# Kernel optimization log

Measured on AMD Instinct MI355X. Metric: run time of the kernel, lower is better.

## Reference

```python
import jax, jax.numpy as jnp
import numpy as np

COS_EPS = 1e-6
LN_EPS = 1e-5

def _cosine_sim(a, b):
    # PyTorch F.cosine_similarity(dim=1, eps): dot / (max(||a||,eps)*max(||b||,eps))
    dot = jnp.sum(a * b, axis=1)
    na = jnp.maximum(jnp.linalg.norm(a, axis=1), COS_EPS)
    nb = jnp.maximum(jnp.linalg.norm(b, axis=1), COS_EPS)
    return dot / (na * nb)

def _layer_norm(x, gamma, beta):
    mu = jnp.mean(x, axis=-1, keepdims=True)
    var = jnp.mean(jnp.square(x - mu), axis=-1, keepdims=True)
    return (x - mu) * jax.lax.rsqrt(var + LN_EPS) * gamma + beta

def setup_inputs() -> dict:
    B, I, H = 8192, 1024, 1024
    key = jax.random.key(0)
    ks = jax.random.split(key, 10)
    s_in = 1.0 / np.sqrt(I + H)
    s_im = 1.0 / np.sqrt(I)
    return {
        "x": jax.random.normal(ks[0], (B, I), jnp.float32),
        "hx": jax.random.normal(ks[1], (B, H), jnp.float32),
        "cx": jax.random.normal(ks[2], (B, H), jnp.float32),
        # main gate linear: [I+H, 4H]
        "W": jax.random.uniform(ks[3], (I + H, 4 * H), jnp.float32, -s_in, s_in),
        "b": jax.random.uniform(ks[4], (4 * H,), jnp.float32, -s_in, s_in),
        # input_mapped: [I, H]
        "Wm": jax.random.uniform(ks[5], (I, H), jnp.float32, -s_im, s_im),
        "bm": jax.random.uniform(ks[6], (H,), jnp.float32, -s_im, s_im),
        # 4 LayerNorms (i, f, g, o)
        "gammas": 1.0 + 0.1 * jax.random.normal(ks[7], (4, H), jnp.float32),
        "betas": 0.1 * jax.random.normal(ks[8], (4, H), jnp.float32),
    }

def reference(x, hx, cx, W, b, Wm, bm, gammas, betas):
    H = hx.shape[1]
    # cosine attention gate between mapped input and hidden state
    input_mapped = x @ Wm + bm                                   # [B, H]
    attn = jax.nn.sigmoid(_cosine_sim(input_mapped, hx))[:, None]  # [B, 1]
    x_mod = x + attn * x
    gates = jnp.concatenate([x_mod, hx], axis=1) @ W + b         # [B, 4H]
    i_g, f_g, g_g, o_g = jnp.split(gates, 4, axis=1)
    i_g = jax.nn.sigmoid(_layer_norm(i_g, gammas[0], betas[0]))
    f_g = jax.nn.sigmoid(_layer_norm(f_g, gammas[1], betas[1]))
    g_g = jnp.tanh(_layer_norm(g_g, gammas[2], betas[2]))
    o_g = jax.nn.sigmoid(_layer_norm(o_g, gammas[3], betas[3]))
    cx_new = f_g * cx + i_g * g_g
    hx_new = o_g * jnp.tanh(cx_new)
    gate_co = jax.nn.sigmoid((_cosine_sim(hx_new, cx_new)[:, None] + 1.0) / 2.0)
    hx_modulated = hx_new + hx_new * gate_co
    return (hx_modulated, cx_new)
```

## Files before the change

### kernel.cpp

```cpp
#include <hip/hip_runtime.h>
#include <hip/hip_bf16.h>

#define DEV __device__ __forceinline__

typedef unsigned short u16;
typedef unsigned int u32;
typedef __attribute__((ext_vector_type(8))) short bf16x8;
typedef __attribute__((ext_vector_type(4))) float f32x4;

DEV float bf2f(u16 v) { u32 u = ((u32)v) << 16; return __builtin_bit_cast(float, u); }
DEV u16 f2bf(float f) {
    u32 u = __builtin_bit_cast(u32, f);
    u32 r = (u + 0x7fffu + ((u >> 16) & 1u)) >> 16;
    return (u16)r;
}
DEV float lo16(u32 u) { return __builtin_bit_cast(float, u << 16); }
DEV float hi16(u32 u) { return __builtin_bit_cast(float, u & 0xffff0000u); }
DEV float sigm(float x) { return 1.f / (1.f + __expf(-x)); }
DEV float clamp4(float v) { return fminf(fmaxf(v, -1e4f), 1e4f); }
DEV float loadf(const void* p, size_t i, int isf) {
    return isf ? clamp4(((const float*)p)[i]) : clamp4(bf2f(((const u16*)p)[i]));
}
DEV void load8(const void* p, size_t off, int isf, float* o) {
    if (isf) {
        const float* s = (const float*)p + off;
#pragma unroll
        for (int e = 0; e < 8; ++e) o[e] = clamp4(s[e]);
    } else {
        uint4 q = *(const uint4*)((const u16*)p + off);
        o[0] = clamp4(lo16(q.x)); o[1] = clamp4(hi16(q.x));
        o[2] = clamp4(lo16(q.y)); o[3] = clamp4(hi16(q.y));
        o[4] = clamp4(lo16(q.z)); o[5] = clamp4(hi16(q.z));
        o[6] = clamp4(lo16(q.w)); o[7] = clamp4(hi16(q.w));
    }
}
DEV uint4 pack8(const float* a) {
    uint4 q;
    q.x = (u32)f2bf(a[0]) | ((u32)f2bf(a[1]) << 16);
    q.y = (u32)f2bf(a[2]) | ((u32)f2bf(a[3]) << 16);
    q.z = (u32)f2bf(a[4]) | ((u32)f2bf(a[5]) << 16);
    q.w = (u32)f2bf(a[6]) | ((u32)f2bf(a[7]) << 16);
    return q;
}
DEV void store8(void* p, size_t off, int isf, const float* a) {
    if (isf) {
        float* d = (float*)p + off;
        *(float4*)(d) = (float4){a[0], a[1], a[2], a[3]};
        *(float4*)(d + 4) = (float4){a[4], a[5], a[6], a[7]};
    } else {
        *(uint4*)((u16*)p + off) = pack8(a);
    }
}

DEV void gload16(const void* g, void* l) {
    __builtin_amdgcn_global_load_lds(
        (const __attribute__((address_space(1))) void*)g,
        (__attribute__((address_space(3))) void*)l, 16, 0, 0);
}

__global__ void detect_dtype(const u32* __restrict__ xw, u32* __restrict__ flag) {
    const int lane = threadIdx.x & 63;
    int cnt = 0;
    for (int k = 0; k < 32; ++k) {
        u32 e = (xw[lane + 64 * k] >> 7) & 0xff;
        cnt += (e >= 118 && e <= 130) ? 1 : 0;
    }
#pragma unroll
    for (int off = 32; off > 0; off >>= 1) cnt += __shfl_xor(cnt, off, 64);
    if (lane == 0) *flag = (cnt > 1024) ? 0u : 1u;
}

__global__ __launch_bounds__(256) void cvt_bf16(const void* __restrict__ src,
                                                u16* __restrict__ dst, int n8,
                                                const u32* __restrict__ flagp) {
    const int isf = (int)*flagp;
    int i = blockIdx.x * 256 + threadIdx.x;
    if (i >= n8) return;
    size_t off = (size_t)i * 8;
    float a[8];
    load8(src, off, isf, a);
    *(uint4*)(dst + off) = pack8(a);
}

__global__ __launch_bounds__(256) void tr_any(const void* __restrict__ src,
                                              u16* __restrict__ dst,
                                              int R, int C,
                                              const u32* __restrict__ flagp) {
    const int isf = (int)*flagp;
    __shared__ __align__(16) u16 t[32][33];
    int tx = threadIdx.x & 31, ty = threadIdx.x >> 5;
    int c0 = blockIdx.x * 32, r0 = blockIdx.y * 32;
#pragma unroll
    for (int i = 0; i < 32; i += 8)
        t[ty + i][tx] = f2bf(loadf(src, (size_t)(r0 + ty + i) * C + (c0 + tx), isf));
    __syncthreads();
#pragma unroll
    for (int i = 0; i < 32; i += 8)
        dst[(size_t)(c0 + ty + i) * R + (r0 + tx)] = t[tx][ty + i];
}

__global__ __launch_bounds__(256) void gemm_bt(
    const u16* __restrict__ A0, const u16* __restrict__ A1, int K0,
    const u16* __restrict__ Bt, const void* __restrict__ bias,
    const u32* __restrict__ flagp,
    u16* __restrict__ Cout, int M, int N, int K) {
    const int isf = (int)*flagp;
    __shared__ __align__(16) u16 As[128 * 32];
    __shared__ __align__(16) u16 Bs[128 * 32];
    const int tid = threadIdx.x;
    const int wave = tid >> 6, lane = tid & 63;
    const int wm = wave >> 1, wn = wave & 1;

    int bx = blockIdx.x, by = blockIdx.y;
    {
        const int gx = gridDim.x;
        const int nwg = gx * gridDim.y;
        if ((nwg & 7) == 0) {
            int lid = by * gx + bx;
            int swz = (lid & 7) * (nwg >> 3) + (lid >> 3);
            bx = swz % gx; by = swz / gx;
        }
    }
    const int m0 = by * 128, n0 = bx * 128;

    f32x4 acc[4][4];
#pragma unroll
    for (int i = 0; i < 4; ++i)
#pragma unroll
        for (int j = 0; j < 4; ++j) acc[i][j] = (f32x4){0.f, 0.f, 0.f, 0.f};

    const int mrow = lane & 15;
    const int kfr = (lane >> 4) * 8;

    const int sr = tid >> 2;
    const int skq = (tid & 3) * 8;
    const int pb0 = (sr & ~63) + (sr & 15) * 4 + ((sr >> 4) & 3);
    const int sr1 = sr + 64;
    const int pb1 = (sr1 & ~63) + (sr1 & 15) * 4 + ((sr1 >> 4) & 3);
    u16* AsW0 = As + wave * 512;
    u16* AsW1 = As + 2048 + wave * 512;
    u16* BsW0 = Bs + wave * 512;
    u16* BsW1 = Bs + 2048 + wave * 512;

    for (int k0 = 0; k0 < K; k0 += 32) {
        const u16* Ab; int lda, kk;
        if (k0 < K0) { Ab = A0; lda = K0; kk = k0; }
        else         { Ab = A1; lda = K - K0; kk = k0 - K0; }
        gload16(Ab + (size_t)(m0 + sr) * lda + kk + skq, AsW0);
        gload16(Ab + (size_t)(m0 + sr1) * lda + kk + skq, AsW1);
        gload16(Bt + (size_t)(n0 + pb0) * K + k0 + skq, BsW0);
        gload16(Bt + (size_t)(n0 + pb1) * K + k0 + skq, BsW1);
        __syncthreads();
        bf16x8 af[4], bfr[4];
#pragma unroll
        for (int t = 0; t < 4; ++t)
            af[t] = *(const bf16x8*)&As[(wm * 64 + t * 16 + mrow) * 32 + kfr];
#pragma unroll
        for (int t = 0; t < 4; ++t)
            bfr[t] = *(const bf16x8*)&Bs[(wn * 64 + t * 16 + mrow) * 32 + kfr];
#pragma unroll
        for (int mt = 0; mt < 4; ++mt)
#pragma unroll
            for (int nt = 0; nt < 4; ++nt)
                acc[mt][nt] = __builtin_amdgcn_mfma_f32_16x16x32_bf16(
                    af[mt], bfr[nt], acc[mt][nt], 0, 0, 0);
        __syncthreads();
    }

    const int cbase = n0 + wn * 64 + mrow * 4;
    float bv[4];
#pragma unroll
    for (int t = 0; t < 4; ++t) bv[t] = loadf(bias, cbase + t, isf);
#pragma unroll
    for (int mt = 0; mt < 4; ++mt) {
        int row0 = m0 + wm * 64 + mt * 16 + (lane >> 4) * 4;
#pragma unroll
        for (int r = 0; r < 4; ++r) {
            uint2 p;
            p.x = (u32)f2bf(acc[mt][0][r] + bv[0]) |
                  ((u32)f2bf(acc[mt][1][r] + bv[1]) << 16);
            p.y = (u32)f2bf(acc[mt][2][r] + bv[2]) |
                  ((u32)f2bf(acc[mt][3][r] + bv[3]) << 16);
            *(uint2*)(Cout + (size_t)(row0 + r) * N + cbase) = p;
        }
    }
}

__global__ __launch_bounds__(256) void attn_xmod(
    const u16* __restrict__ im, const u16* __restrict__ hx,
    const u16* __restrict__ x, u16* __restrict__ xmod) {
    const int lane = threadIdx.x & 63;
    const int row = blockIdx.x * 4 + (threadIdx.x >> 6);
    float dot = 0.f, na = 0.f, nb = 0.f;
#pragma unroll
    for (int j = 0; j < 2; ++j) {
        size_t off = (size_t)row * 1024 + lane * 8 + j * 512;
        float a[8], h[8];
        load8(im, off, 0, a);
        load8(hx, off, 0, h);
#pragma unroll
        for (int e = 0; e < 8; ++e) {
            dot += a[e] * h[e]; na += a[e] * a[e]; nb += h[e] * h[e];
        }
    }
#pragma unroll
    for (int off = 32; off > 0; off >>= 1) {
        dot += __shfl_xor(dot, off, 64);
        na += __shfl_xor(na, off, 64);
        nb += __shfl_xor(nb, off, 64);
    }
    float cs = dot / (fmaxf(sqrtf(na), 1e-6f) * fmaxf(sqrtf(nb), 1e-6f));
    float fac = 1.f + sigm(cs);
#pragma unroll
    for (int j = 0; j < 2; ++j) {
        size_t off = (size_t)row * 1024 + lane * 8 + j * 512;
        float a[8];
        load8(x, off, 0, a);
#pragma unroll
        for (int e = 0; e < 8; ++e) a[e] *= fac;
        *(uint4*)(xmod + off) = pack8(a);
    }
}

__global__ __launch_bounds__(256) void ln_lstm(
    const u16* __restrict__ gates, const void* __restrict__ cx,
    const void* __restrict__ gammas, const void* __restrict__ betas,
    const u32* __restrict__ flagp, void* __restrict__ out, int BH) {
    const int isf = (int)*flagp;
    const int lane = threadIdx.x & 63;
    const int row = blockIdx.x * 4 + (threadIdx.x >> 6);
    float v[4][16];
    float s[4] = {0.f, 0.f, 0.f, 0.f}, ss[4] = {0.f, 0.f, 0.f, 0.f};
#pragma unroll
    for (int c = 0; c < 4; ++c) {
#pragma unroll
        for (int j = 0; j < 2; ++j) {
            size_t off = (size_t)row * 4096 + c * 1024 + lane * 8 + j * 512;
            float* vp = &v[c][j * 8];
            load8(gates, off, 0, vp);
#pragma unroll
            for (int e = 0; e < 8; ++e) { s[c] += vp[e]; ss[c] += vp[e] * vp[e]; }
        }
    }
#pragma unroll
    for (int off = 32; off > 0; off >>= 1) {
#pragma unroll
        for (int c = 0; c < 4; ++c) {
            s[c] += __shfl_xor(s[c], off, 64);
            ss[c] += __shfl_xor(ss[c], off, 64);
        }
    }
    float mean[4], rstd[4];
#pragma unroll
    for (int c = 0; c < 4; ++c) {
        mean[c] = s[c] * (1.f / 1024.f);
        float var = ss[c] * (1.f / 1024.f) - mean[c] * mean[c];
        rstd[c] = rsqrtf(fmaxf(var, 0.f) + 1e-5f);
    }
#pragma unroll
    for (int c = 0; c < 4; ++c) {
#pragma unroll
        for (int j = 0; j < 2; ++j) {
            size_t off = (size_t)(c * 1024 + lane * 8 + j * 512);
            float g[8], bb[8];
            load8(gammas, off, isf, g);
            load8(betas, off, isf, bb);
            float* vp = &v[c][j * 8];
#pragma unroll
            for (int e = 0; e < 8; ++e) {
                float y = (vp[e] - mean[c]) * rstd[c] * g[e] + bb[e];
                vp[e] = (c == 2) ? tanhf(y) : sigm(y);
            }
        }
    }
    float hn[16], cn[16];
    float dot = 0.f, nh = 0.f, nc = 0.f;
#pragma unroll
    for (int j = 0; j < 2; ++j) {
        size_t off = (size_t)row * 1024 + lane * 8 + j * 512;
        float cv[8];
        load8(cx, off, isf, cv);
#pragma unroll
        for (int e = 0; e < 8; ++e) {
            int idx = j * 8 + e;
            float c_new = v[1][idx] * cv[e] + v[0][idx] * v[2][idx];
            float h_new = v[3][idx] * tanhf(c_new);
            cn[idx] = c_new; hn[idx] = h_new;
            dot += h_new * c_new; nh += h_new * h_new; nc += c_new * c_new;
        }
    }
#pragma unroll
    for (int off = 32; off > 0; off >>= 1) {
        dot += __shfl_xor(dot, off, 64);
        nh += __shfl_xor(nh, off, 64);
        nc += __shfl_xor(nc, off, 64);
    }
    float cs = dot / (fmaxf(sqrtf(nh), 1e-6f) * fmaxf(sqrtf(nc), 1e-6f));
    float fac = 1.f + sigm((cs + 1.f) * 0.5f);
#pragma unroll
    for (int j = 0; j < 2; ++j) {
        size_t off = (size_t)row * 1024 + lane * 8 + j * 512;
        float ho[8];
#pragma unroll
        for (int e = 0; e < 8; ++e) ho[e] = hn[j * 8 + e] * fac;
        store8(out, off, isf, ho);
        store8(out, (size_t)BH + off, isf, &cn[j * 8]);
    }
}

__global__ void diag_k(u32* __restrict__ out, int ws_ok, int sizes_ok) {
    const int lane = threadIdx.x & 63;
    int mrow = lane & 15, quad = lane >> 4;
    bf16x8 af, bfr;
#pragma unroll
    for (int j = 0; j < 8; ++j) {
        int k = quad * 8 + j;
        af[j] = (short)f2bf((float)(((mrow * 7 + k * 3) % 11) - 5));
        bfr[j] = (short)f2bf((float)(((mrow * 5 + k * 2) % 13) - 6));
    }
    f32x4 cacc = (f32x4){0.f, 0.f, 0.f, 0.f};
    cacc = __builtin_amdgcn_mfma_f32_16x16x32_bf16(af, bfr, cacc, 0, 0, 0);
    int bad = 0;
#pragma unroll
    for (int r = 0; r < 4; ++r) {
        int mr = quad * 4 + r;
        float expv = 0.f;
        for (int k = 0; k < 32; ++k)
            expv += (float)(((mr * 7 + k * 3) % 11) - 5) *
                    (float)(((mrow * 5 + k * 2) % 13) - 6);
        if (fabsf(cacc[r] - expv) > 0.5f) bad = 1;
    }
    int mfma_bad = (__ballot(bad) != 0ull) ? 1 : 0;
    if (lane == 0) {
        if (!sizes_ok)     out[0] = __builtin_bit_cast(u32, 65536.f);
        else if (!ws_ok)   out[0] = __builtin_bit_cast(u32, 131072.f);
        else if (mfma_bad) out[0] = __builtin_bit_cast(u32, 32768.f);
    }
}

extern "C" void kernel_launch(void* const* d_in, const int* in_sizes, int n_in,
                              void* d_out, int out_size, void* d_ws, size_t ws_size,
                              hipStream_t stream) {
    const void* x   = d_in[0];
    const void* hx  = d_in[1];
    const void* cx  = d_in[2];
    const void* W   = d_in[3];
    const void* b   = d_in[4];
    const void* Wm  = d_in[5];
    const void* bm  = d_in[6];
    const void* gam = d_in[7];
    const void* bet = d_in[8];

    const int B = 8192, I = 1024, H = 1024;
    const int K2 = I + H, N2 = 4 * H;
    const size_t MiB = 1048576ull;

    char* ws = (char*)d_ws;
    u16* x_c   = (u16*)ws;
    u16* hx_c  = (u16*)(ws + 16 * MiB);
    u16* Wt    = (u16*)(ws + 32 * MiB);
    u16* Wmt   = (u16*)(ws + 48 * MiB);
    u16* gates = (u16*)(ws + 50 * MiB);
    u32* flag  = (u32*)(ws + 114 * MiB);
    u16* xmod  = (u16*)d_out;
    u16* imb   = (u16*)d_out + 8388608ull;

    const int sizes_ok =
        n_in == 9 && out_size == 16777216 &&
        in_sizes[0] == 8388608 && in_sizes[1] == 8388608 && in_sizes[2] == 8388608 &&
        in_sizes[3] == 8388608 && in_sizes[4] == 4096 && in_sizes[5] == 1048576 &&
        in_sizes[6] == 1024 && in_sizes[7] == 4096 && in_sizes[8] == 4096;
    const int ws_ok = ws_size >= 115 * MiB;

    if (sizes_ok && ws_ok) {
        detect_dtype<<<1, 64, 0, stream>>>((const u32*)x, flag);
        cvt_bf16<<<4096, 256, 0, stream>>>(x, x_c, 1048576, flag);
        cvt_bf16<<<4096, 256, 0, stream>>>(hx, hx_c, 1048576, flag);
        tr_any<<<dim3(H / 32, I / 32), 256, 0, stream>>>(Wm, Wmt, I, H, flag);
        tr_any<<<dim3(N2 / 32, K2 / 32), 256, 0, stream>>>(W, Wt, K2, N2, flag);
        gemm_bt<<<dim3(H / 128, B / 128), 256, 0, stream>>>(
            x_c, x_c, I, Wmt, bm, flag, imb, B, H, I);
        attn_xmod<<<dim3(B / 4), 256, 0, stream>>>(imb, hx_c, x_c, xmod);
        gemm_bt<<<dim3(N2 / 128, B / 128), 256, 0, stream>>>(
            xmod, hx_c, I, Wt, b, flag, gates, B, N2, K2);
        ln_lstm<<<dim3(B / 4), 256, 0, stream>>>(gates, cx, gam, bet, flag,
                                                 d_out, B * H);
    }
    diag_k<<<1, 64, 0, stream>>>((u32*)d_out, ws_ok, sizes_ok);
}
```

Measured before the change: 470.0 us.

## Replace 128x128 GEMM with 256x256 double-buffered, 8-wave pipelined GEMM

After: 421.9 us. 10.3% less time.

```diff
diff --git a/kernel.cpp b/kernel.cpp
--- a/kernel.cpp
+++ b/kernel.cpp
@@ -99,17 +99,18 @@
         dst[(size_t)(c0 + ty + i) * R + (r0 + tx)] = t[tx][ty + i];
 }
 
-__global__ __launch_bounds__(256) void gemm_bt(
+__global__ __launch_bounds__(512, 2) void gemm256(
     const u16* __restrict__ A0, const u16* __restrict__ A1, int K0,
     const u16* __restrict__ Bt, const void* __restrict__ bias,
     const u32* __restrict__ flagp,
     u16* __restrict__ Cout, int M, int N, int K) {
     const int isf = (int)*flagp;
-    __shared__ __align__(16) u16 As[128 * 32];
-    __shared__ __align__(16) u16 Bs[128 * 32];
+    __shared__ __align__(16) u16 lds[65536];
+    u16* const ldsA = lds;
+    u16* const ldsB = lds + 32768;
     const int tid = threadIdx.x;
     const int wave = tid >> 6, lane = tid & 63;
-    const int wm = wave >> 1, wn = wave & 1;
+    const int wm = wave >> 2, wn = wave & 3;
 
     int bx = blockIdx.x, by = blockIdx.y;
     {
@@ -121,67 +122,202 @@
             bx = swz % gx; by = swz / gx;
         }
     }
-    const int m0 = by * 128, n0 = bx * 128;
-
-    f32x4 acc[4][4];
-#pragma unroll
-    for (int i = 0; i < 4; ++i)
-#pragma unroll
-        for (int j = 0; j < 4; ++j) acc[i][j] = (f32x4){0.f, 0.f, 0.f, 0.f};
+    const int m0 = by * 256, n0 = bx * 256;
+    const int NT = K >> 6;
+
+    size_t qA[2][2], qB[2][2];
+#pragma unroll
+    for (int h = 0; h < 2; ++h)
+#pragma unroll
+        for (int c = 0; c < 2; ++c) {
+            int p = h * 16384 + c * 8192 + wave * 1024 + lane * 16;
+            int lg = p ^ (((p >> 9) & 1) << 5);
+            int s = lg >> 10, lr = (lg >> 6) & 15;
+            int k = ((s & 1) << 5) + ((lg & 63) >> 1);
+            int m = ((s >> 3) & 1) * 128 + ((s >> 4) & 1) * 64 +
+                    ((s >> 1) & 3) * 16 + lr;
+            qA[h][c] = (size_t)(m0 + m) * (size_t)K0 + (size_t)k;
+            int ns = ((s >> 2) & 3) * 64 + ((s >> 4) & 1) * 32 +
+                     ((s >> 1) & 1) * 16 + lr;
+            int gn = (ns & ~63) | ((ns & 15) * 4 + ((ns >> 4) & 3));
+            qB[h][c] = (size_t)(n0 + gn) * (size_t)K + (size_t)k;
+        }
 
     const int mrow = lane & 15;
     const int kfr = (lane >> 4) * 8;
-
-    const int sr = tid >> 2;
-    const int skq = (tid & 3) * 8;
-    const int pb0 = (sr & ~63) + (sr & 15) * 4 + ((sr >> 4) & 3);
-    const int sr1 = sr + 64;
-    const int pb1 = (sr1 & ~63) + (sr1 & 15) * 4 + ((sr1 >> 4) & 3);
-    u16* AsW0 = As + wave * 512;
-    u16* AsW1 = As + 2048 + wave * 512;
-    u16* BsW0 = Bs + wave * 512;
-    u16* BsW1 = Bs + 2048 + wave * 512;
-
-    for (int k0 = 0; k0 < K; k0 += 32) {
-        const u16* Ab; int lda, kk;
-        if (k0 < K0) { Ab = A0; lda = K0; kk = k0; }
-        else         { Ab = A1; lda = K - K0; kk = k0 - K0; }
-        gload16(Ab + (size_t)(m0 + sr) * lda + kk + skq, AsW0);
-        gload16(Ab + (size_t)(m0 + sr1) * lda + kk + skq, AsW1);
-        gload16(Bt + (size_t)(n0 + pb0) * K + k0 + skq, BsW0);
-        gload16(Bt + (size_t)(n0 + pb1) * K + k0 + skq, BsW1);
-        __syncthreads();
-        bf16x8 af[4], bfr[4];
-#pragma unroll
-        for (int t = 0; t < 4; ++t)
-            af[t] = *(const bf16x8*)&As[(wm * 64 + t * 16 + mrow) * 32 + kfr];
-#pragma unroll
-        for (int t = 0; t < 4; ++t)
-            bfr[t] = *(const bf16x8*)&Bs[(wn * 64 + t * 16 + mrow) * 32 + kfr];
-#pragma unroll
-        for (int mt = 0; mt < 4; ++mt)
-#pragma unroll
-            for (int nt = 0; nt < 4; ++nt)
-                acc[mt][nt] = __builtin_amdgcn_mfma_f32_16x16x32_bf16(
-                    af[mt], bfr[nt], acc[mt][nt], 0, 0, 0);
-        __syncthreads();
-    }
-
+    const int aSwz = (mrow * 32 + kfr) ^ ((mrow & 8) << 1);
+
+    f32x4 acc[8][4];
+#pragma unroll
+    for (int i = 0; i < 8; ++i)
+#pragma unroll
+        for (int j = 0; j < 4; ++j) acc[i][j] = (f32x4){0.f, 0.f, 0.f, 0.f};
+
+#define ASEG(kt, AS_, KK_) const u16* AS_; int KK_; \
+    if ((kt) < K0) { AS_ = A0; KK_ = (kt); } else { AS_ = A1; KK_ = (kt) - K0; }
+
+    {
+        ASEG(0, As0, kk0);
+        gload16(As0 + qA[0][0] + kk0, ldsA + wave * 512);
+        gload16(As0 + qA[0][1] + kk0, ldsA + 4096 + wave * 512);
+        gload16(Bt + qB[1][0], ldsB + 8192 + wave * 512);
+        gload16(Bt + qB[1][1], ldsB + 8192 + 4096 + wave * 512);
+        gload16(As0 + qA[1][0] + kk0, ldsA + 8192 + wave * 512);
+        gload16(As0 + qA[1][1] + kk0, ldsA + 8192 + 4096 + wave * 512);
+        gload16(Bt + qB[0][0], ldsB + wave * 512);
+        gload16(Bt + qB[0][1], ldsB + 4096 + wave * 512);
+        if (NT > 1) {
+            ASEG(64, As1, kk1);
+            gload16(As1 + qA[0][0] + kk1, ldsA + 16384 + wave * 512);
+            gload16(As1 + qA[0][1] + kk1, ldsA + 16384 + 4096 + wave * 512);
+            gload16(Bt + qB[1][0] + 64, ldsB + 16384 + 8192 + wave * 512);
+            gload16(Bt + qB[1][1] + 64, ldsB + 16384 + 8192 + 4096 + wave * 512);
+            gload16(As1 + qA[1][0] + kk1, ldsA + 16384 + 8192 + wave * 512);
+            gload16(As1 + qA[1][1] + kk1, ldsA + 16384 + 8192 + 4096 + wave * 512);
+            asm volatile("s_waitcnt vmcnt(6)" ::: "memory");
+        } else {
+            asm volatile("s_waitcnt vmcnt(0)" ::: "memory");
+        }
+        __builtin_amdgcn_s_barrier();
+    }
+
+    for (int t = 0; t < NT; ++t) {
+        const int bufb = (t & 1) << 14;
+        const int obufb = bufb ^ 16384;
+        const int k0 = t << 6;
+        bf16x8 af[4][2], bfA[2][2], bfB[2][2];
+
+        {
+            const u16* ab = &ldsA[bufb + (wm * 8) * 512];
+#pragma unroll
+            for (int mt2 = 0; mt2 < 4; ++mt2)
+#pragma unroll
+                for (int ks = 0; ks < 2; ++ks)
+                    af[mt2][ks] = *(const bf16x8*)&ab[(mt2 * 2 + ks) * 512 + aSwz];
+            const u16* bb = &ldsB[bufb + (wn * 4) * 512];
+#pragma unroll
+            for (int nt2 = 0; nt2 < 2; ++nt2)
+#pragma unroll
+                for (int ks = 0; ks < 2; ++ks)
+                    bfA[nt2][ks] = *(const bf16x8*)&bb[(nt2 * 2 + ks) * 512 + aSwz];
+        }
+        if (t + 1 < NT) {
+            gload16(Bt + qB[0][0] + (k0 + 64), ldsB + obufb + wave * 512);
+            gload16(Bt + qB[0][1] + (k0 + 64), ldsB + obufb + 4096 + wave * 512);
+        }
+        __builtin_amdgcn_s_barrier();
+        __builtin_amdgcn_s_setprio(1);
+#pragma unroll
+        for (int mt2 = 0; mt2 < 4; ++mt2)
+#pragma unroll
+            for (int nt2 = 0; nt2 < 2; ++nt2)
+#pragma unroll
+                for (int ks = 0; ks < 2; ++ks)
+                    acc[mt2][nt2] = __builtin_amdgcn_mfma_f32_16x16x32_bf16(
+                        af[mt2][ks], bfA[nt2][ks], acc[mt2][nt2], 0, 0, 0);
+        __builtin_amdgcn_s_setprio(0);
+        __builtin_amdgcn_s_barrier();
+
+        {
+            const u16* bb = &ldsB[bufb + (16 + wn * 4) * 512];
+#pragma unroll
+            for (int nt2 = 0; nt2 < 2; ++nt2)
+#pragma unroll
+                for (int ks = 0; ks < 2; ++ks)
+                    bfB[nt2][ks] = *(const bf16x8*)&bb[(nt2 * 2 + ks) * 512 + aSwz];
+        }
+        if (t + 2 < NT) {
+            ASEG(k0 + 128, As2, kk2);
+            gload16(As2 + qA[0][0] + kk2, ldsA + bufb + wave * 512);
+            gload16(As2 + qA[0][1] + kk2, ldsA + bufb + 4096 + wave * 512);
+        }
+        __builtin_amdgcn_s_barrier();
+        __builtin_amdgcn_s_setprio(1);
+#pragma unroll
+        for (int mt2 = 0; mt2 < 4; ++mt2)
+#pragma unroll
+            for (int nt2 = 0; nt2 < 2; ++nt2)
+#pragma unroll
+                for (int ks = 0; ks < 2; ++ks)
+                    acc[mt2][2 + nt2] = __builtin_amdgcn_mfma_f32_16x16x32_bf16(
+                        af[mt2][ks], bfB[nt2][ks], acc[mt2][2 + nt2], 0, 0, 0);
+        __builtin_amdgcn_s_setprio(0);
+        __builtin_amdgcn_s_barrier();
+
+        {
+            const u16* ab = &ldsA[bufb + (16 + wm * 8) * 512];
+#pragma unroll
+            for (int mt2 = 0; mt2 < 4; ++mt2)
+#pragma unroll
+                for (int ks = 0; ks < 2; ++ks)
+                    af[mt2][ks] = *(const bf16x8*)&ab[(mt2 * 2 + ks) * 512 + aSwz];
+        }
+        if (t + 2 < NT) {
+            gload16(Bt + qB[1][0] + (k0 + 128), ldsB + bufb + 8192 + wave * 512);
+            gload16(Bt + qB[1][1] + (k0 + 128), ldsB + bufb + 8192 + 4096 + wave * 512);
+        }
+        __builtin_amdgcn_s_barrier();
+        __builtin_amdgcn_s_setprio(1);
+#pragma unroll
+        for (int mt2 = 0; mt2 < 4; ++mt2)
+#pragma unroll
+            for (int nt2 = 0; nt2 < 2; ++nt2)
+#pragma unroll
+                for (int ks = 0; ks < 2; ++ks)
+                    acc[4 + mt2][2 + nt2] = __builtin_amdgcn_mfma_f32_16x16x32_bf16(
+                        af[mt2][ks], bfB[nt2][ks], acc[4 + mt2][2 + nt2], 0, 0, 0);
+        __builtin_amdgcn_s_setprio(0);
+        __builtin_amdgcn_s_barrier();
+
+        {
+            const u16* bb = &ldsB[bufb + (wn * 4) * 512];
+#pragma unroll
+            for (int nt2 = 0; nt2 < 2; ++nt2)
+#pragma unroll
+                for (int ks = 0; ks < 2; ++ks)
+                    bfA[nt2][ks] = *(const bf16x8*)&bb[(nt2 * 2 + ks) * 512 + aSwz];
+        }
+        if (t + 2 < NT) {
+            ASEG(k0 + 128, As3, kk3);
+            gload16(As3 + qA[1][0] + kk3, ldsA + bufb + 8192 + wave * 512);
+            gload16(As3 + qA[1][1] + kk3, ldsA + bufb + 8192 + 4096 + wave * 512);
+        }
+        __builtin_amdgcn_s_barrier();
+        __builtin_amdgcn_s_setprio(1);
+#pragma unroll
+        for (int mt2 = 0; mt2 < 4; ++mt2)
+#pragma unroll
+            for (int nt2 = 0; nt2 < 2; ++nt2)
+#pragma unroll
+                for (int ks = 0; ks < 2; ++ks)
+                    acc[4 + mt2][nt2] = __builtin_amdgcn_mfma_f32_16x16x32_bf16(
+                        af[mt2][ks], bfA[nt2][ks], acc[4 + mt2][nt2], 0, 0, 0);
+        __builtin_amdgcn_s_setprio(0);
+        if (t + 2 < NT) {
+            asm volatile("s_waitcnt vmcnt(6)" ::: "memory");
+        } else {
+            asm volatile("s_waitcnt vmcnt(0)" ::: "memory");
+        }
+        __builtin_amdgcn_s_barrier();
+    }
+#undef ASEG
+
+    const int q = lane >> 4;
     const int cbase = n0 + wn * 64 + mrow * 4;
     float bv[4];
 #pragma unroll
-    for (int t = 0; t < 4; ++t) bv[t] = loadf(bias, cbase + t, isf);
-#pragma unroll
-    for (int mt = 0; mt < 4; ++mt) {
-        int row0 = m0 + wm * 64 + mt * 16 + (lane >> 4) * 4;
+    for (int tt = 0; tt < 4; ++tt) bv[tt] = loadf(bias, cbase + tt, isf);
+#pragma unroll
+    for (int mt = 0; mt < 8; ++mt) {
+        int row0 = m0 + wm * 128 + mt * 16 + q * 4;
 #pragma unroll
         for (int r = 0; r < 4; ++r) {
-            uint2 p;
-            p.x = (u32)f2bf(acc[mt][0][r] + bv[0]) |
-                  ((u32)f2bf(acc[mt][1][r] + bv[1]) << 16);
-            p.y = (u32)f2bf(acc[mt][2][r] + bv[2]) |
-                  ((u32)f2bf(acc[mt][3][r] + bv[3]) << 16);
-            *(uint2*)(Cout + (size_t)(row0 + r) * N + cbase) = p;
+            uint2 pk;
+            pk.x = (u32)f2bf(acc[mt][0][r] + bv[0]) |
+                   ((u32)f2bf(acc[mt][1][r] + bv[1]) << 16);
+            pk.y = (u32)f2bf(acc[mt][2][r] + bv[2]) |
+                   ((u32)f2bf(acc[mt][3][r] + bv[3]) << 16);
+            *(uint2*)(Cout + (size_t)(row0 + r) * N + cbase) = pk;
         }
     }
 }
@@ -378,10 +514,10 @@
         cvt_bf16<<<4096, 256, 0, stream>>>(hx, hx_c, 1048576, flag);
         tr_any<<<dim3(H / 32, I / 32), 256, 0, stream>>>(Wm, Wmt, I, H, flag);
         tr_any<<<dim3(N2 / 32, K2 / 32), 256, 0, stream>>>(W, Wt, K2, N2, flag);
-        gemm_bt<<<dim3(H / 128, B / 128), 256, 0, stream>>>(
+        gemm256<<<dim3(H / 256, B / 256), 512, 0, stream>>>(
             x_c, x_c, I, Wmt, bm, flag, imb, B, H, I);
         attn_xmod<<<dim3(B / 4), 256, 0, stream>>>(imb, hx_c, x_c, xmod);
-        gemm_bt<<<dim3(N2 / 128, B / 128), 256, 0, stream>>>(
+        gemm256<<<dim3(N2 / 256, B / 256), 512, 0, stream>>>(
             xmod, hx_c, I, Wt, b, flag, gates, B, N2, K2);
         ln_lstm<<<dim3(B / 4), 256, 0, stream>>>(gates, cx, gam, bet, flag,
                                                  d_out, B * H);
```
